# Performance work log

Hardware: AMD Instinct MI355X
Metric: run time of the kernel (lower is better)

Reference implementation:

```python
import jax, jax.numpy as jnp
import numpy as np

N = 50000        # nodes
E = 800_000      # edges (avg degree 16)
D_IN, D_HID, D_OUT = 512, 512, 256
P_DROP = 0.5


def setup_inputs() -> dict:
    key = jax.random.key(0)
    k0, k1, k2, k3 = jax.random.split(key, 4)
    x = jax.random.normal(k0, (N, D_IN), dtype=jnp.float32)
    edge_index = jax.random.randint(k1, (2, E), 0, N, dtype=jnp.int64)
    W1 = jax.random.normal(k2, (D_HID, D_IN), dtype=jnp.float32) * 0.02
    b1 = jnp.zeros((D_HID,), dtype=jnp.float32)
    W2 = jax.random.normal(k3, (D_OUT, D_HID), dtype=jnp.float32) * 0.02
    b2 = jnp.zeros((D_OUT,), dtype=jnp.float32)
    return {"x": x, "edge_index": edge_index, "W1": W1, "b1": b1, "W2": W2, "b2": b2}


def _gcn_norm(edge_index, n):
    # add self loops, then symmetric GCN normalization: D^-1/2 (A+I) D^-1/2
    src, dst = edge_index[0], edge_index[1]
    loops = jnp.arange(n, dtype=src.dtype)
    src = jnp.concatenate([src, loops])
    dst = jnp.concatenate([dst, loops])
    deg = jax.ops.segment_sum(jnp.ones_like(src, dtype=jnp.float32), dst, num_segments=n)
    dinv = jax.lax.rsqrt(deg)  # deg >= 1 because of self loops
    norm = dinv[src] * dinv[dst]  # [E+N]
    return src, dst, norm


def _propagate(x, src, dst, norm):
    # out[i] = sum_{(j->i)} norm_e * x[j]
    return jax.ops.segment_sum(x[src] * norm[:, None], dst, num_segments=x.shape[0])


def reference(x, edge_index, W1, b1, W2, b2):
    src, dst, norm = _gcn_norm(edge_index, x.shape[0])
    # SGConv layer 1 (K=1): propagate then linear
    h = _propagate(x, src, dst, norm) @ W1.T + b1
    h = jax.nn.relu(h)
    # F.dropout(p) with training=True default -> deterministic fixed-key mask here
    keep = jax.random.bernoulli(jax.random.key(42), 1.0 - P_DROP, h.shape)
    embedding = jnp.where(keep, h / (1.0 - P_DROP), 0.0)
    # SGConv layer 2
    out = _propagate(embedding, src, dst, norm) @ W2.T + b2
    return embedding, out
```

## Files before the change

### kernel.cpp

```cpp
#include <hip/hip_runtime.h>

typedef unsigned short u16t;
typedef __attribute__((ext_vector_type(8))) short short8;
typedef __attribute__((ext_vector_type(4))) short short4v;
typedef __attribute__((ext_vector_type(4))) float f32x4;
typedef __attribute__((ext_vector_type(4))) unsigned short u16x4;

__device__ __forceinline__ float bf2f(short b) {
  return __uint_as_float(((unsigned)(unsigned short)b) << 16);
}
__device__ __forceinline__ u16t f2bf(float f) {
  unsigned u = __float_as_uint(f);
  u += 0x7FFFu + ((u >> 16) & 1u);
  return (u16t)(u >> 16);
}

__device__ __forceinline__ bool keep_mask(unsigned flat) {
  const unsigned k0 = 0u, k1 = 42u;
  const unsigned k2 = k0 ^ k1 ^ 0x1BD11BDAu;
  unsigned x0 = 0u + k0;
  unsigned x1 = flat + k1;
#define TF_R(r) { x0 += x1; x1 = (x1 << r) | (x1 >> (32 - r)); x1 ^= x0; }
  TF_R(13) TF_R(15) TF_R(26) TF_R(6)  x0 += k1; x1 += k2 + 1u;
  TF_R(17) TF_R(29) TF_R(16) TF_R(24) x0 += k2; x1 += k0 + 2u;
  TF_R(13) TF_R(15) TF_R(26) TF_R(6)  x0 += k0; x1 += k1 + 3u;
  TF_R(17) TF_R(29) TF_R(16) TF_R(24) x0 += k1; x1 += k2 + 4u;
  TF_R(13) TF_R(15) TF_R(26) TF_R(6)  x0 += k2; x1 += k0 + 5u;
#undef TF_R
  return ((x0 ^ x1) >> 31) == 0u;
}

__device__ __forceinline__ void load_lds16(const u16t* g, u16t* l) {
  __builtin_amdgcn_global_load_lds((__attribute__((address_space(1))) void*)g,
                                   (__attribute__((address_space(3))) void*)l,
                                   16, 0, 0);
}

__global__ void cvt_bf16(const float* __restrict__ s, u16t* __restrict__ d, int n) {
  int i = (blockIdx.x * 256 + threadIdx.x) * 4;
  if (i < n) {
    f32x4 v = *(const f32x4*)&s[i];
    u16x4 o = { f2bf(v.x), f2bf(v.y), f2bf(v.z), f2bf(v.w) };
    *(u16x4*)&d[i] = o;
  }
}

__global__ void count_edges(const int* __restrict__ dst, int E, int* __restrict__ cnt) {
  int e = blockIdx.x * 256 + threadIdx.x;
  if (e < E) atomicAdd(&cnt[dst[e]], 1);
}

__global__ __launch_bounds__(256) void rowp_build(const int* __restrict__ cnt,
    int* __restrict__ rowp, int* __restrict__ cursor, float* __restrict__ dinv,
    int* __restrict__ gctr, int n) {
  __shared__ int sd[256];
  __shared__ int sbase;
  const int tid = threadIdx.x;
  const int i = blockIdx.x * 256 + tid;
  int c = (i < n) ? cnt[i] : 0;
  int v = c;
  sd[tid] = v;
  __syncthreads();
  for (int o = 1; o < 256; o <<= 1) {
    int t = (tid >= o) ? sd[tid - o] : 0;
    __syncthreads();
    v += t;
    sd[tid] = v;
    __syncthreads();
  }
  if (tid == 255) sbase = atomicAdd(gctr, v);
  __syncthreads();
  if (i < n) {
    int start = sbase + v - c;
    rowp[i] = start;
    cursor[i] = start;
    dinv[i] = rsqrtf((float)(c + 1));
  }
}

__global__ void fill_csr(const int* __restrict__ src, const int* __restrict__ dst, int E,
                         int* __restrict__ cursor, int* __restrict__ col) {
  int e = blockIdx.x * 256 + threadIdx.x;
  if (e < E) {
    int d = dst[e];
    int pos = atomicAdd(&cursor[d], 1);
    col[pos] = src[e];
  }
}

__global__ __launch_bounds__(256) void gemm_bt(const u16t* __restrict__ A,
                                               const u16t* __restrict__ B,
                                               u16t* __restrict__ C,
                                               int K, int Ncols) {
  __shared__ __align__(16) u16t lA[128 * 32];
  __shared__ __align__(16) u16t lB[128 * 32];
  const int tid = threadIdx.x;
  const int wave = tid >> 6, lane = tid & 63;
  const int wm = (wave & 1) * 64, wn = (wave >> 1) * 64;
  const int lrow = lane & 15, lq = lane >> 4;
  const u16t* Ab = A + (size_t)blockIdx.x * 128 * K;
  const u16t* Bb = B + (size_t)blockIdx.y * 128 * K;
  const int r0 = tid >> 2, c0 = (tid & 3) * 8;
  const int ldsOff = __builtin_amdgcn_readfirstlane((tid >> 6) * 512);

  f32x4 acc[4][4];
  const f32x4 zero = {0.f, 0.f, 0.f, 0.f};
#pragma unroll
  for (int mi = 0; mi < 4; ++mi)
#pragma unroll
    for (int ni = 0; ni < 4; ++ni) acc[mi][ni] = zero;

  for (int kt = 0; kt < K; kt += 32) {
    __syncthreads();
    load_lds16(Ab + (size_t)r0 * K + kt + c0, &lA[ldsOff]);
    load_lds16(Ab + (size_t)(r0 + 64) * K + kt + c0, &lA[2048 + ldsOff]);
    load_lds16(Bb + (size_t)r0 * K + kt + c0, &lB[ldsOff]);
    load_lds16(Bb + (size_t)(r0 + 64) * K + kt + c0, &lB[2048 + ldsOff]);
    __syncthreads();
    short8 af[4], bfr[4];
#pragma unroll
    for (int mi = 0; mi < 4; ++mi)
      af[mi] = *(const short8*)&lA[(wm + mi * 16 + lrow) * 32 + lq * 8];
#pragma unroll
    for (int ni = 0; ni < 4; ++ni)
      bfr[ni] = *(const short8*)&lB[(wn + ni * 16 + lrow) * 32 + lq * 8];
#pragma unroll
    for (int mi = 0; mi < 4; ++mi)
#pragma unroll
      for (int ni = 0; ni < 4; ++ni)
        acc[mi][ni] = __builtin_amdgcn_mfma_f32_16x16x32_bf16(af[mi], bfr[ni], acc[mi][ni], 0, 0, 0);
  }

  const size_t crow = (size_t)blockIdx.x * 128 + wm + lq * 4;
  const int ccol = blockIdx.y * 128 + wn + lrow;
#pragma unroll
  for (int mi = 0; mi < 4; ++mi)
#pragma unroll
    for (int r = 0; r < 4; ++r)
#pragma unroll
      for (int ni = 0; ni < 4; ++ni)
        C[(crow + mi * 16 + r) * Ncols + ccol + ni * 16] = f2bf(acc[mi][ni][r]);
}

__global__ __launch_bounds__(256) void prop1_kernel(const u16t* __restrict__ y1,
    const int* __restrict__ col, const int* __restrict__ rowp, const int* __restrict__ rowend,
    const float* __restrict__ dinv, const float* __restrict__ b1,
    float* __restrict__ embf, u16t* __restrict__ embb, int n) {
  const int lane = threadIdx.x & 63;
  const int i = blockIdx.x * 4 + (threadIdx.x >> 6);
  if (i >= n) return;
  const int f = lane * 8;
  const float di = dinv[i];
  float acc[8];
  short8 v = *(const short8*)&y1[(size_t)i * 512 + f];
#pragma unroll
  for (int j = 0; j < 8; ++j) acc[j] = di * bf2f(v[j]);
  int e = rowp[i];
  const int e1 = rowend[i];
  for (; e + 4 <= e1; e += 4) {
    const int s0 = col[e], s1 = col[e + 1], s2 = col[e + 2], s3 = col[e + 3];
    const float w0 = dinv[s0], w1 = dinv[s1], w2 = dinv[s2], w3 = dinv[s3];
    short8 u0 = *(const short8*)&y1[(size_t)s0 * 512 + f];
    short8 u1 = *(const short8*)&y1[(size_t)s1 * 512 + f];
    short8 u2 = *(const short8*)&y1[(size_t)s2 * 512 + f];
    short8 u3 = *(const short8*)&y1[(size_t)s3 * 512 + f];
#pragma unroll
    for (int j = 0; j < 8; ++j) acc[j] += w0 * bf2f(u0[j]);
#pragma unroll
    for (int j = 0; j < 8; ++j) acc[j] += w1 * bf2f(u1[j]);
#pragma unroll
    for (int j = 0; j < 8; ++j) acc[j] += w2 * bf2f(u2[j]);
#pragma unroll
    for (int j = 0; j < 8; ++j) acc[j] += w3 * bf2f(u3[j]);
  }
  for (; e < e1; ++e) {
    const int s = col[e];
    const float w = dinv[s];
    short8 u = *(const short8*)&y1[(size_t)s * 512 + f];
#pragma unroll
    for (int j = 0; j < 8; ++j) acc[j] += w * bf2f(u[j]);
  }
  const unsigned flat = (unsigned)i * 512u + (unsigned)f;
  f32x4 o0, o1;
  short8 ob;
#pragma unroll
  for (int j = 0; j < 8; ++j) {
    float h = di * acc[j] + b1[f + j];
    h = fmaxf(h, 0.f);
    float eb = keep_mask(flat + (unsigned)j) ? 2.f * h : 0.f;
    if (j < 4) o0[j] = eb; else o1[j - 4] = eb;
    ob[j] = (short)f2bf(eb);
  }
  *(f32x4*)&embf[(size_t)i * 512 + f] = o0;
  *(f32x4*)&embf[(size_t)i * 512 + f + 4] = o1;
  *(short8*)&embb[(size_t)i * 512 + f] = ob;
}

__global__ __launch_bounds__(256) void prop2_kernel(const u16t* __restrict__ z,
    const int* __restrict__ col, const int* __restrict__ rowp, const int* __restrict__ rowend,
    const float* __restrict__ dinv, const float* __restrict__ b2,
    float* __restrict__ outp, int n) {
  const int lane = threadIdx.x & 63;
  const int i = blockIdx.x * 4 + (threadIdx.x >> 6);
  if (i >= n) return;
  const int f = lane * 4;
  const float di = dinv[i];
  float acc[4];
  short4v v = *(const short4v*)&z[(size_t)i * 256 + f];
#pragma unroll
  for (int j = 0; j < 4; ++j) acc[j] = di * bf2f(v[j]);
  int e = rowp[i];
  const int e1 = rowend[i];
  for (; e + 4 <= e1; e += 4) {
    const int s0 = col[e], s1 = col[e + 1], s2 = col[e + 2], s3 = col[e + 3];
    const float w0 = dinv[s0], w1 = dinv[s1], w2 = dinv[s2], w3 = dinv[s3];
    short4v u0 = *(const short4v*)&z[(size_t)s0 * 256 + f];
    short4v u1 = *(const short4v*)&z[(size_t)s1 * 256 + f];
    short4v u2 = *(const short4v*)&z[(size_t)s2 * 256 + f];
    short4v u3 = *(const short4v*)&z[(size_t)s3 * 256 + f];
#pragma unroll
    for (int j = 0; j < 4; ++j) acc[j] += w0 * bf2f(u0[j]);
#pragma unroll
    for (int j = 0; j < 4; ++j) acc[j] += w1 * bf2f(u1[j]);
#pragma unroll
    for (int j = 0; j < 4; ++j) acc[j] += w2 * bf2f(u2[j]);
#pragma unroll
    for (int j = 0; j < 4; ++j) acc[j] += w3 * bf2f(u3[j]);
  }
  for (; e < e1; ++e) {
    const int s = col[e];
    const float w = dinv[s];
    short4v u = *(const short4v*)&z[(size_t)s * 256 + f];
#pragma unroll
    for (int j = 0; j < 4; ++j) acc[j] += w * bf2f(u[j]);
  }
  f32x4 o;
#pragma unroll
  for (int j = 0; j < 4; ++j) o[j] = di * acc[j] + b2[f + j];
  *(f32x4*)&outp[(size_t)i * 256 + f] = o;
}

extern "C" void kernel_launch(void* const* d_in, const int* in_sizes, int n_in,
                              void* d_out, int out_size, void* d_ws, size_t ws_size,
                              hipStream_t stream) {
  (void)n_in; (void)out_size; (void)ws_size;
  const float* x  = (const float*)d_in[0];
  const int*   ei = (const int*)d_in[1];
  const float* W1 = (const float*)d_in[2];
  const float* b1 = (const float*)d_in[3];
  const float* W2 = (const float*)d_in[4];
  const float* b2 = (const float*)d_in[5];

  const int Nn = in_sizes[0] / 512;
  const int E  = in_sizes[1] / 2;
  const int Mpad = ((Nn + 127) / 128) * 128;
  const int K = 512;

  char* ws = (char*)d_ws;
  size_t off = 0;
  auto take = [&](size_t bytes) -> char* {
    char* p = ws + off;
    off += (bytes + 255) & ~(size_t)255;
    return p;
  };
  u16t* xb   = (u16t*)take((size_t)Mpad * 512 * 2);
  u16t* y1b  = (u16t*)take((size_t)Mpad * 512 * 2);
  u16t* W1b  = (u16t*)take((size_t)512 * 512 * 2);
  u16t* W2b  = (u16t*)take((size_t)256 * 512 * 2);
  int*   cnt    = (int*)take((size_t)(Nn + 1) * 4);
  int*   rowp   = (int*)take((size_t)Nn * 4);
  int*   cursor = (int*)take((size_t)Nn * 4);
  float* dinv   = (float*)take((size_t)Nn * 4);
  int*   colA   = (int*)take((size_t)E * 4);

  float* embf = (float*)d_out;
  float* outf = (float*)d_out + (size_t)Nn * 512;

  hipMemsetAsync(cnt, 0, (size_t)(Nn + 1) * 4, stream);

  const int n1 = Nn * 512;
  cvt_bf16<<<(n1 / 4 + 255) / 256, 256, 0, stream>>>(x, xb, n1);
  cvt_bf16<<<(512 * 512 / 4 + 255) / 256, 256, 0, stream>>>(W1, W1b, 512 * 512);
  cvt_bf16<<<(256 * 512 / 4 + 255) / 256, 256, 0, stream>>>(W2, W2b, 256 * 512);

  count_edges<<<(E + 255) / 256, 256, 0, stream>>>(ei + E, E, cnt);
  rowp_build<<<(Nn + 255) / 256, 256, 0, stream>>>(cnt, rowp, cursor, dinv, cnt + Nn, Nn);
  fill_csr<<<(E + 255) / 256, 256, 0, stream>>>(ei, ei + E, E, cursor, colA);

  dim3 g1(Mpad / 128, 4);
  gemm_bt<<<g1, 256, 0, stream>>>(xb, W1b, y1b, K, 512);
  prop1_kernel<<<(Nn + 3) / 4, 256, 0, stream>>>(y1b, colA, rowp, cursor, dinv, b1,
                                                 embf, xb , Nn);

  u16t* zb = y1b;
  dim3 g2(Mpad / 128, 2);
  gemm_bt<<<g2, 256, 0, stream>>>(xb, W2b, zb, K, 256);
  prop2_kernel<<<(Nn + 3) / 4, 256, 0, stream>>>(zb, colA, rowp, cursor, dinv, b2, outf, Nn);
}
```

Measured before the change: 590.9 us.

## Swap GEMM grid order, deepen prop1 gather unroll, widen prop2 to 16B loads

After: 591.4 us. No clear change (+0.1%).

```diff
diff --git a/kernel.cpp b/kernel.cpp
--- a/kernel.cpp
+++ b/kernel.cpp
@@ -2,7 +2,6 @@
 
 typedef unsigned short u16t;
 typedef __attribute__((ext_vector_type(8))) short short8;
-typedef __attribute__((ext_vector_type(4))) short short4v;
 typedef __attribute__((ext_vector_type(4))) float f32x4;
 typedef __attribute__((ext_vector_type(4))) unsigned short u16x4;
 
@@ -98,8 +97,8 @@
   const int wave = tid >> 6, lane = tid & 63;
   const int wm = (wave & 1) * 64, wn = (wave >> 1) * 64;
   const int lrow = lane & 15, lq = lane >> 4;
-  const u16t* Ab = A + (size_t)blockIdx.x * 128 * K;
-  const u16t* Bb = B + (size_t)blockIdx.y * 128 * K;
+  const u16t* Ab = A + (size_t)blockIdx.y * 128 * K;
+  const u16t* Bb = B + (size_t)blockIdx.x * 128 * K;
   const int r0 = tid >> 2, c0 = (tid & 3) * 8;
   const int ldsOff = __builtin_amdgcn_readfirstlane((tid >> 6) * 512);
 
@@ -131,8 +130,8 @@
         acc[mi][ni] = __builtin_amdgcn_mfma_f32_16x16x32_bf16(af[mi], bfr[ni], acc[mi][ni], 0, 0, 0);
   }
 
-  const size_t crow = (size_t)blockIdx.x * 128 + wm + lq * 4;
-  const int ccol = blockIdx.y * 128 + wn + lrow;
+  const size_t crow = (size_t)blockIdx.y * 128 + wm + lq * 4;
+  const int ccol = blockIdx.x * 128 + wn + lrow;
 #pragma unroll
   for (int mi = 0; mi < 4; ++mi)
 #pragma unroll
@@ -157,21 +156,35 @@
   for (int j = 0; j < 8; ++j) acc[j] = di * bf2f(v[j]);
   int e = rowp[i];
   const int e1 = rowend[i];
+  for (; e + 8 <= e1; e += 8) {
+    int s[8];
+    float w[8];
+    short8 u[8];
+#pragma unroll
+    for (int q = 0; q < 8; ++q) s[q] = col[e + q];
+#pragma unroll
+    for (int q = 0; q < 8; ++q) w[q] = dinv[s[q]];
+#pragma unroll
+    for (int q = 0; q < 8; ++q) u[q] = *(const short8*)&y1[(size_t)s[q] * 512 + f];
+#pragma unroll
+    for (int q = 0; q < 8; ++q)
+#pragma unroll
+      for (int j = 0; j < 8; ++j) acc[j] += w[q] * bf2f(u[q][j]);
+  }
   for (; e + 4 <= e1; e += 4) {
-    const int s0 = col[e], s1 = col[e + 1], s2 = col[e + 2], s3 = col[e + 3];
-    const float w0 = dinv[s0], w1 = dinv[s1], w2 = dinv[s2], w3 = dinv[s3];
-    short8 u0 = *(const short8*)&y1[(size_t)s0 * 512 + f];
-    short8 u1 = *(const short8*)&y1[(size_t)s1 * 512 + f];
-    short8 u2 = *(const short8*)&y1[(size_t)s2 * 512 + f];
-    short8 u3 = *(const short8*)&y1[(size_t)s3 * 512 + f];
-#pragma unroll
-    for (int j = 0; j < 8; ++j) acc[j] += w0 * bf2f(u0[j]);
-#pragma unroll
-    for (int j = 0; j < 8; ++j) acc[j] += w1 * bf2f(u1[j]);
-#pragma unroll
-    for (int j = 0; j < 8; ++j) acc[j] += w2 * bf2f(u2[j]);
-#pragma unroll
-    for (int j = 0; j < 8; ++j) acc[j] += w3 * bf2f(u3[j]);
+    int s[4];
+    float w[4];
+    short8 u[4];
+#pragma unroll
+    for (int q = 0; q < 4; ++q) s[q] = col[e + q];
+#pragma unroll
+    for (int q = 0; q < 4; ++q) w[q] = dinv[s[q]];
+#pragma unroll
+    for (int q = 0; q < 4; ++q) u[q] = *(const short8*)&y1[(size_t)s[q] * 512 + f];
+#pragma unroll
+    for (int q = 0; q < 4; ++q)
+#pragma unroll
+      for (int j = 0; j < 8; ++j) acc[j] += w[q] * bf2f(u[q][j]);
   }
   for (; e < e1; ++e) {
     const int s = col[e];
@@ -200,44 +213,47 @@
     const int* __restrict__ col, const int* __restrict__ rowp, const int* __restrict__ rowend,
     const float* __restrict__ dinv, const float* __restrict__ b2,
     float* __restrict__ outp, int n) {
-  const int lane = threadIdx.x & 63;
-  const int i = blockIdx.x * 4 + (threadIdx.x >> 6);
+  const int h = threadIdx.x & 31;
+  const int i = blockIdx.x * 8 + (threadIdx.x >> 5);
   if (i >= n) return;
-  const int f = lane * 4;
+  const int f = h * 8;
   const float di = dinv[i];
-  float acc[4];
-  short4v v = *(const short4v*)&z[(size_t)i * 256 + f];
-#pragma unroll
-  for (int j = 0; j < 4; ++j) acc[j] = di * bf2f(v[j]);
+  float acc[8];
+  short8 v = *(const short8*)&z[(size_t)i * 256 + f];
+#pragma unroll
+  for (int j = 0; j < 8; ++j) acc[j] = di * bf2f(v[j]);
   int e = rowp[i];
   const int e1 = rowend[i];
   for (; e + 4 <= e1; e += 4) {
-    const int s0 = col[e], s1 = col[e + 1], s2 = col[e + 2], s3 = col[e + 3];
-    const float w0 = dinv[s0], w1 = dinv[s1], w2 = dinv[s2], w3 = dinv[s3];
-    short4v u0 = *(const short4v*)&z[(size_t)s0 * 256 + f];
-    short4v u1 = *(const short4v*)&z[(size_t)s1 * 256 + f];
-    short4v u2 = *(const short4v*)&z[(size_t)s2 * 256 + f];
-    short4v u3 = *(const short4v*)&z[(size_t)s3 * 256 + f];
-#pragma unroll
-    for (int j = 0; j < 4; ++j) acc[j] += w0 * bf2f(u0[j]);
-#pragma unroll
-    for (int j = 0; j < 4; ++j) acc[j] += w1 * bf2f(u1[j]);
-#pragma unroll
-    for (int j = 0; j < 4; ++j) acc[j] += w2 * bf2f(u2[j]);
-#pragma unroll
-    for (int j = 0; j < 4; ++j) acc[j] += w3 * bf2f(u3[j]);
+    int s[4];
+    float w[4];
+    short8 u[4];
+#pragma unroll
+    for (int q = 0; q < 4; ++q) s[q] = col[e + q];
+#pragma unroll
+    for (int q = 0; q < 4; ++q) w[q] = dinv[s[q]];
+#pragma unroll
+    for (int q = 0; q < 4; ++q) u[q] = *(const short8*)&z[(size_t)s[q] * 256 + f];
+#pragma unroll
+    for (int q = 0; q < 4; ++q)
+#pragma unroll
+      for (int j = 0; j < 8; ++j) acc[j] += w[q] * bf2f(u[q][j]);
   }
   for (; e < e1; ++e) {
     const int s = col[e];
     const float w = dinv[s];
-    short4v u = *(const short4v*)&z[(size_t)s * 256 + f];
-#pragma unroll
-    for (int j = 0; j < 4; ++j) acc[j] += w * bf2f(u[j]);
-  }
-  f32x4 o;
-#pragma unroll
-  for (int j = 0; j < 4; ++j) o[j] = di * acc[j] + b2[f + j];
-  *(f32x4*)&outp[(size_t)i * 256 + f] = o;
+    short8 u = *(const short8*)&z[(size_t)s * 256 + f];
+#pragma unroll
+    for (int j = 0; j < 8; ++j) acc[j] += w * bf2f(u[j]);
+  }
+  f32x4 o0, o1;
+#pragma unroll
+  for (int j = 0; j < 8; ++j) {
+    float r = di * acc[j] + b2[f + j];
+    if (j < 4) o0[j] = r; else o1[j - 4] = r;
+  }
+  *(f32x4*)&outp[(size_t)i * 256 + f] = o0;
+  *(f32x4*)&outp[(size_t)i * 256 + f + 4] = o1;
 }
 
 extern "C" void kernel_launch(void* const* d_in, const int* in_sizes, int n_in,
@@ -287,13 +303,13 @@
   rowp_build<<<(Nn + 255) / 256, 256, 0, stream>>>(cnt, rowp, cursor, dinv, cnt + Nn, Nn);
   fill_csr<<<(E + 255) / 256, 256, 0, stream>>>(ei, ei + E, E, cursor, colA);
 
-  dim3 g1(Mpad / 128, 4);
+  dim3 g1(512 / 128, Mpad / 128);
   gemm_bt<<<g1, 256, 0, stream>>>(xb, W1b, y1b, K, 512);
   prop1_kernel<<<(Nn + 3) / 4, 256, 0, stream>>>(y1b, colA, rowp, cursor, dinv, b1,
                                                  embf, xb , Nn);
 
   u16t* zb = y1b;
-  dim3 g2(Mpad / 128, 2);
+  dim3 g2(256 / 128, Mpad / 128);
   gemm_bt<<<g2, 256, 0, stream>>>(xb, W2b, zb, K, 256);
-  prop2_kernel<<<(Nn + 3) / 4, 256, 0, stream>>>(zb, colA, rowp, cursor, dinv, b2, outf, Nn);
-}
+  prop2_kernel<<<(Nn + 7) / 8, 256, 0, stream>>>(zb, colA, rowp, cursor, dinv, b2, outf, Nn);
+}
```
